# Kernel optimization log

Hardware: AMD Instinct MI355X
Metric: run time of the kernel (lower is better)

## Reference

```python
import jax, jax.numpy as jnp
import numpy as np
from jax import lax

B, S, D, H = 512, 120, 216, 1024
MAX_LEN = 24


def setup_inputs() -> dict:
    key = jax.random.key(0)
    ks = jax.random.split(key, 8)
    u = lambda k, shape: jax.random.uniform(k, shape, jnp.float32, -0.08, 0.08)  # init_weights
    return {
        "src": jax.random.normal(ks[0], (B, S, D), jnp.float32),
        "W_ih": u(ks[1], (4 * H, D)),
        "W_hh": u(ks[2], (4 * H, H)),
        "b_ih": u(ks[3], (4 * H,)),
        "b_hh": u(ks[4], (4 * H,)),
        "W_out": u(ks[5], (D, H)),
        "b_out": u(ks[6], (D,)),
        "max_len": MAX_LEN,
    }


def _lstm_cell(x, h, c, W_ih, W_hh, b):
    # PyTorch gate order: i, f, g, o
    gates = x @ W_ih.T + h @ W_hh.T + b  # (B, 4H)
    i, f, g, o = jnp.split(gates, 4, axis=-1)
    c_new = jax.nn.sigmoid(f) * c + jax.nn.sigmoid(i) * jnp.tanh(g)
    h_new = jax.nn.sigmoid(o) * jnp.tanh(c_new)
    return h_new, c_new


def reference(src, W_ih, W_hh, b_ih, b_hh, W_out, b_out, max_len):
    # Eval-mode forward: dropout off; encoder teacher-forced over src;
    b = b_ih + b_hh
    src_t = jnp.swapaxes(src, 0, 1)  # (S, B, D)
    Bsz = src.shape[0]
    Hd = W_hh.shape[1]
    h0 = jnp.zeros((Bsz, Hd), src.dtype)
    c0 = jnp.zeros((Bsz, Hd), src.dtype)

    def enc_step(carry, x_t):
        h, c = carry
        h, c = _lstm_cell(x_t, h, c, W_ih, W_hh, b)
        return (h, c), None

    (h, c), _ = lax.scan(enc_step, (h0, c0), src_t)

    def dec_step(carry, _):
        h, c, inp = carry
        h, c = _lstm_cell(inp, h, c, W_ih, W_hh, b)
        y = h @ W_out.T + b_out  # project_to_output
        return (h, c, y), y

    (_, _, _), ys = lax.scan(dec_step, (h, c, src_t[-1]), None, length=max_len)
    return jnp.swapaxes(ys, 0, 1)  # (B, max_len, D)
```

## Files before the change

### kernel.cpp

```cpp
#include <hip/hip_runtime.h>
#include <cstdint>
#include <cstddef>

#define B_SZ 512
#define S_SZ 120
#define D_SZ 216
#define H_SZ 1024
#define NG   4096
#define DP   256
#define KENC 1280
#define TMAX 24

#define BM 64
#define BN 128
#define BK 64

using bf16_t = __bf16;
using bf16x8 = __attribute__((ext_vector_type(8))) __bf16;
using f32x4  = __attribute__((ext_vector_type(4))) float;

__device__ __forceinline__ void gload16(const void* g, void* l) {
  __builtin_amdgcn_global_load_lds(
      (const __attribute__((address_space(1))) void*)g,
      (__attribute__((address_space(3))) void*)l, 16, 0, 0);
}

__device__ __forceinline__ float fsigmoid(float x) {
  x = fminf(fmaxf(x, -30.f), 30.f);
  return 1.f / (1.f + __expf(-x));
}
__device__ __forceinline__ float ftanh(float x) {
  x = fminf(fmaxf(x, -15.f), 15.f);
  float e = __expf(2.f * x);
  return (e - 1.f) / (e + 1.f);
}

#define BUFB 24576
struct __align__(16) Smem {
  union {
    bf16_t stage[3][(BM + BN) * BK];
    float gate[BM * 129];
  };
};

template <int EPI>
__global__ __launch_bounds__(256, 1) void gemm_step(
    const bf16_t* __restrict__ A1, int sA1, int n1,
    const bf16_t* __restrict__ A2, int sA2, int n2,
    const bf16_t* __restrict__ W, int sW,
    const float* __restrict__ bias,
    float* __restrict__ cbuf, bf16_t* __restrict__ hout,
    const float* __restrict__ addm, bf16_t* __restrict__ outb,
    float* __restrict__ outf)
{
  __shared__ Smem sm;
  const int t    = threadIdx.x;
  const int m0   = blockIdx.y * BM;
  const int n0   = blockIdx.x * BN;
  const int lane = t & 63;
  const int wv   = t >> 6;
  const int wm   = wv >> 1, wn = wv & 1;
  const int fr   = lane & 15;
  const int fq   = lane >> 4;

  f32x4 acc[2][4] = {};

  float bias4[4];
  if (EPI == 1 || EPI == 3) {
#pragma unroll
    for (int j = 0; j < 4; ++j) {
      int col = n0 + wn * 64 + j * 16 + fr;
      bias4[j] = (EPI == 3 && col >= D_SZ) ? 0.f : bias[col];
    }
  }

  const int r0   = t >> 3;
  const int gcol = (((t & 7) ^ (r0 & 7)) * 8);
  char* ldsbase  = (char*)&sm.stage[0][0];
  const int wofs = wv * 1024;

  const bf16_t* pA1 = A1 ? A1 : A2;
  const bf16_t* pA2 = A2 ? A2 : A1;
  const bf16_t* a1p0 = pA1 + (size_t)(m0 + r0) * sA1 + gcol;
  const bf16_t* a1p1 = pA1 + (size_t)(m0 + r0 + 32) * sA1 + gcol;
  const bf16_t* a2p0 = pA2 + (size_t)(m0 + r0) * sA2 + gcol;
  const bf16_t* a2p1 = pA2 + (size_t)(m0 + r0 + 32) * sA2 + gcol;
  const bf16_t* wp0  = W + (size_t)(n0 + r0) * sW + gcol;
  const bf16_t* wp1  = W + (size_t)(n0 + r0 + 32) * sW + gcol;
  const bf16_t* wp2  = W + (size_t)(n0 + r0 + 64) * sW + gcol;
  const bf16_t* wp3  = W + (size_t)(n0 + r0 + 96) * sW + gcol;

  const int nTot = n1 + n2;

  auto stage = [&](int j, int bf) {
    char* Ab = ldsbase + bf * BUFB + wofs;
    char* Bb = ldsbase + bf * BUFB + 8192 + wofs;
    const int k = j * BK;
    const bf16_t *a0, *a1;
    if (j < n1) { a0 = a1p0 + k; a1 = a1p1 + k; }
    else { const int k2 = k - n1 * BK; a0 = a2p0 + k2; a1 = a2p1 + k2; }
    gload16(a0, Ab);
    gload16(a1, Ab + 4096);
    gload16(wp0 + k, Bb);
    gload16(wp1 + k, Bb + 4096);
    gload16(wp2 + k, Bb + 8192);
    gload16(wp3 + k, Bb + 12288);
  };

  const int swz  = fr & 7;
  const int co0  = ((fq) ^ swz) * 16;
  const int co1  = ((4 + fq) ^ swz) * 16;
  const int arow0 = (wm * 32 + fr) * 128;
  const int arow1 = (wm * 32 + 16 + fr) * 128;
  const int brow  = (wn * 64 + fr) * 128;

  auto compute = [&](int bf) {
    const char* Ab = ldsbase + bf * BUFB;
    const char* Bb = Ab + 8192;
#pragma unroll
    for (int kk = 0; kk < 2; ++kk) {
      const int co = kk ? co1 : co0;
      bf16x8 av0 = *(const bf16x8*)(Ab + arow0 + co);
      bf16x8 av1 = *(const bf16x8*)(Ab + arow1 + co);
      bf16x8 bv[4];
#pragma unroll
      for (int j = 0; j < 4; ++j)
        bv[j] = *(const bf16x8*)(Bb + brow + j * 2048 + co);
#pragma unroll
      for (int j = 0; j < 4; ++j) {
        acc[0][j] = __builtin_amdgcn_mfma_f32_16x16x32_bf16(av0, bv[j], acc[0][j], 0, 0, 0);
        acc[1][j] = __builtin_amdgcn_mfma_f32_16x16x32_bf16(av1, bv[j], acc[1][j], 0, 0, 0);
      }
    }
  };

  stage(0, 0);
  if (nTot > 1) stage(1, 1);
  int cb = 0, sb = 2;
  for (int it = 0; it < nTot; ++it) {
    if (it == nTot - 1) {
      asm volatile("s_waitcnt vmcnt(0)" ::: "memory");
    } else {
      asm volatile("s_waitcnt vmcnt(6)" ::: "memory");
    }
    __builtin_amdgcn_s_barrier();
    if (it + 2 < nTot) stage(it + 2, sb);
    sb = (sb == 2) ? 0 : sb + 1;
    compute(cb);
    cb = (cb == 2) ? 0 : cb + 1;
  }
  __syncthreads();

  if (EPI == 1) {
#pragma unroll
    for (int i = 0; i < 2; ++i)
#pragma unroll
      for (int j = 0; j < 4; ++j)
#pragma unroll
        for (int v = 0; v < 4; ++v) {
          int row = wm * 32 + i * 16 + fq * 4 + v;
          int col = wn * 64 + j * 16 + fr;
          sm.gate[row * 129 + col] = acc[i][j][v] + bias4[j];
        }
    __syncthreads();
    const int u0 = n0 >> 2;
#pragma unroll
    for (int itc = 0; itc < 8; ++itc) {
      int ci = itc * 256 + t;
      int brw = ci >> 5;
      int ju  = ci & 31;
      const float* gp = &sm.gate[brw * 129 + ju * 4];
      float iv = fsigmoid(gp[0]);
      float fv = fsigmoid(gp[1]);
      float gv = ftanh(gp[2]);
      float ov = fsigmoid(gp[3]);
      size_t cix = (size_t)(m0 + brw) * H_SZ + (u0 + ju);
      float cn = fv * cbuf[cix] + iv * gv;
      cbuf[cix] = cn;
      hout[cix] = (bf16_t)(ov * ftanh(cn));
    }
  }

  if (EPI == 2) {
#pragma unroll
    for (int i = 0; i < 2; ++i)
#pragma unroll
      for (int j = 0; j < 4; ++j)
#pragma unroll
        for (int v = 0; v < 4; ++v) {
          int gr = m0 + wm * 32 + i * 16 + fq * 4 + v;
          int gc = n0 + wn * 64 + j * 16 + fr;
          int orig = (gr & 3) * H_SZ + (gr >> 2);
          float val = acc[i][j][v] + addm[(size_t)orig * H_SZ + gc];
          outb[(size_t)gr * H_SZ + gc] = (bf16_t)val;
        }
  }

  if (EPI == 3) {
#pragma unroll
    for (int i = 0; i < 2; ++i)
#pragma unroll
      for (int j = 0; j < 4; ++j)
#pragma unroll
        for (int v = 0; v < 4; ++v) {
          int m = m0 + wm * 32 + i * 16 + fq * 4 + v;
          int n = n0 + wn * 64 + j * 16 + fr;
          if (n < D_SZ) {
            int ts = m >> 9;
            int bb = m & 511;
            outf[((size_t)bb * TMAX + ts) * D_SZ + n] = acc[i][j][v] + bias4[j];
          }
        }
  }
}

__global__ void k_convert_src(const float* __restrict__ src, bf16_t* __restrict__ dst) {
  int idx = blockIdx.x * 256 + threadIdx.x;
  int total = S_SZ * B_SZ * DP;
  if (idx >= total) return;
  int d = idx % DP;
  int r = idx / DP;
  int b = r % B_SZ;
  int tt = r / B_SZ;
  float v = (d < D_SZ) ? src[((size_t)b * S_SZ + tt) * D_SZ + d] : 0.f;
  dst[idx] = (bf16_t)v;
}

__global__ void k_build_wcat(const float* __restrict__ Wih, const float* __restrict__ Whh,
                             bf16_t* __restrict__ Wcat) {
  int idx = blockIdx.x * 256 + threadIdx.x;
  if (idx >= NG * KENC) return;
  int k = idx % KENC;
  int r = idx / KENC;
  int o = (r & 3) * H_SZ + (r >> 2);
  float v;
  if (k < D_SZ)      v = Wih[(size_t)o * D_SZ + k];
  else if (k < DP)   v = 0.f;
  else               v = Whh[(size_t)o * H_SZ + (k - DP)];
  Wcat[idx] = (bf16_t)v;
}

__global__ void k_build_wout(const float* __restrict__ Wout, bf16_t* __restrict__ WoutB,
                             bf16_t* __restrict__ WoutT) {
  int idx = blockIdx.x * 256 + threadIdx.x;
  if (idx < 256 * H_SZ) {
    int h = idx % H_SZ, d = idx / H_SZ;
    WoutB[idx] = (bf16_t)((d < D_SZ) ? Wout[(size_t)d * H_SZ + h] : 0.f);
  }
  if (idx < H_SZ * DP) {
    int d = idx % DP, h = idx / DP;
    WoutT[idx] = (bf16_t)((d < D_SZ) ? Wout[(size_t)d * H_SZ + h] : 0.f);
  }
}

__global__ void k_build_bias(const float* __restrict__ bih, const float* __restrict__ bhh,
                             const float* __restrict__ Wih, const float* __restrict__ bout,
                             float* __restrict__ biasE, float* __restrict__ biasD) {
  int r = blockIdx.x * 256 + threadIdx.x;
  if (r >= NG) return;
  int o = (r & 3) * H_SZ + (r >> 2);
  float be = bih[o] + bhh[o];
  biasE[r] = be;
  float s = 0.f;
  const float* wr = Wih + (size_t)o * D_SZ;
  for (int d = 0; d < D_SZ; ++d) s += wr[d] * bout[d];
  biasD[r] = be + s;
}

extern "C" void kernel_launch(void* const* d_in, const int* in_sizes, int n_in,
                              void* d_out, int out_size, void* d_ws, size_t ws_size,
                              hipStream_t stream) {
  const float* src  = (const float*)d_in[0];
  const float* Wih  = (const float*)d_in[1];
  const float* Whh  = (const float*)d_in[2];
  const float* bih  = (const float*)d_in[3];
  const float* bhh  = (const float*)d_in[4];
  const float* Wout = (const float*)d_in[5];
  const float* bout = (const float*)d_in[6];

  char* ws = (char*)d_ws;
  size_t off = 0;
  auto alloc = [&](size_t bytes) {
    void* p = ws + off;
    off = (off + bytes + 255) & ~(size_t)255;
    return p;
  };
  bf16_t* srcbf = (bf16_t*)alloc((size_t)S_SZ * B_SZ * DP * 2);
  bf16_t* Wcat  = (bf16_t*)alloc((size_t)NG * KENC * 2);
  bf16_t* Wdec  = (bf16_t*)alloc((size_t)NG * H_SZ * 2);
  bf16_t* WoutB = (bf16_t*)alloc((size_t)256 * H_SZ * 2);
  bf16_t* WoutT = (bf16_t*)alloc((size_t)H_SZ * DP * 2);
  float*  biasE = (float*)alloc((size_t)NG * 4);
  float*  biasD = (float*)alloc((size_t)NG * 4);
  float*  cbuf  = (float*)alloc((size_t)B_SZ * H_SZ * 4);
  bf16_t* hP0   = (bf16_t*)alloc((size_t)B_SZ * H_SZ * 2);
  bf16_t* hP1   = (bf16_t*)alloc((size_t)B_SZ * H_SZ * 2);
  bf16_t* Hs    = (bf16_t*)alloc((size_t)TMAX * B_SZ * H_SZ * 2);

  hipMemsetAsync(cbuf, 0, (size_t)B_SZ * H_SZ * 4, stream);
  hipMemsetAsync(hP0, 0, (size_t)B_SZ * H_SZ * 2, stream);

  k_convert_src<<<(S_SZ * B_SZ * DP + 255) / 256, 256, 0, stream>>>(src, srcbf);
  k_build_wcat<<<(NG * KENC + 255) / 256, 256, 0, stream>>>(Wih, Whh, Wcat);
  k_build_wout<<<1024, 256, 0, stream>>>(Wout, WoutB, WoutT);
  k_build_bias<<<(NG + 255) / 256, 256, 0, stream>>>(bih, bhh, Wih, bout, biasE, biasD);

  gemm_step<2><<<dim3(H_SZ / BN, NG / BM), 256, 0, stream>>>(
      Wcat, KENC, DP / BK, nullptr, 0, 0, WoutT, DP,
      nullptr, nullptr, nullptr, Whh, Wdec, nullptr);

  const bf16_t* hprev = hP0;
  for (int s = 0; s < 144; ++s) {
    bf16_t* hnext;
    if (s < 120) hnext = (hprev == hP0) ? hP1 : hP0;
    else         hnext = Hs + (size_t)(s - 120) * B_SZ * H_SZ;
    if (s <= 120) {
      int xi = (s <= 119) ? s : 119;
      gemm_step<1><<<dim3(NG / BN, B_SZ / BM), 256, 0, stream>>>(
          srcbf + (size_t)xi * B_SZ * DP, DP, DP / BK,
          hprev, H_SZ, H_SZ / BK,
          Wcat, KENC, biasE, cbuf, hnext,
          nullptr, nullptr, nullptr);
    } else {
      gemm_step<1><<<dim3(NG / BN, B_SZ / BM), 256, 0, stream>>>(
          nullptr, 0, 0, hprev, H_SZ, H_SZ / BK,
          Wdec, H_SZ, biasD, cbuf, hnext,
          nullptr, nullptr, nullptr);
    }
    hprev = hnext;
  }

  gemm_step<3><<<dim3(2, (TMAX * B_SZ) / BM), 256, 0, stream>>>(
      nullptr, 0, 0, Hs, H_SZ, H_SZ / BK, WoutB, H_SZ,
      bout, nullptr, nullptr, nullptr, nullptr, (float*)d_out);
}
```

Baseline: 2.018 ms.

## Fuse recurrent LSTM steps into one persistent cooperative kernel with grid barrier

Replaces 144 per-timestep GEMM+cell launches with a single persistent cooperative kernel of 256 blocks that loops over all timesteps. A global atomic-counter barrier separates steps. The hidden state is stored with system-coherent flags and loaded bypassing caches so it is visible across blocks. This removes kernel launch and drain overhead per step, at the cost of spin-wait barrier latency and uncached h loads.

```diff
diff --git a/kernel.cpp b/kernel.cpp
--- a/kernel.cpp
+++ b/kernel.cpp
@@ -24,6 +24,11 @@
       (const __attribute__((address_space(1))) void*)g,
       (__attribute__((address_space(3))) void*)l, 16, 0, 0);
 }
+__device__ __forceinline__ void gload16c(const void* g, void* l) {
+  __builtin_amdgcn_global_load_lds(
+      (const __attribute__((address_space(1))) void*)g,
+      (__attribute__((address_space(3))) void*)l, 16, 0, 0x11);
+}
 
 __device__ __forceinline__ float fsigmoid(float x) {
   x = fminf(fmaxf(x, -30.f), 30.f);
@@ -42,6 +47,172 @@
     float gate[BM * 129];
   };
 };
+
+__global__ __launch_bounds__(256, 1) void lstm_chain(
+    const bf16_t* __restrict__ srcbf,
+    const bf16_t* __restrict__ Wcat,
+    const bf16_t* __restrict__ Wdec,
+    const float* __restrict__ biasE,
+    const float* __restrict__ biasD,
+    float* __restrict__ cbuf,
+    bf16_t* __restrict__ hA,
+    bf16_t* __restrict__ hB,
+    bf16_t* __restrict__ Hs,
+    unsigned* __restrict__ bar)
+{
+  __shared__ Smem sm;
+  const int t    = threadIdx.x;
+  const int bid  = blockIdx.x;
+  const int n0   = (bid & 31) * BN;
+  const int m0   = (bid >> 5) * BM;
+  const int lane = t & 63;
+  const int wv   = t >> 6;
+  const int wm   = wv >> 1, wn = wv & 1;
+  const int fr   = lane & 15;
+  const int fq   = lane >> 4;
+
+  const int r0   = t >> 3;
+  const int gcol = (((t & 7) ^ (r0 & 7)) * 8);
+  char* ldsbase  = (char*)&sm.stage[0][0];
+  const int wofs = wv * 1024;
+
+  const int swz  = fr & 7;
+  const int co0  = ((fq) ^ swz) * 16;
+  const int co1  = ((4 + fq) ^ swz) * 16;
+  const int arow0 = (wm * 32 + fr) * 128;
+  const int arow1 = (wm * 32 + 16 + fr) * 128;
+  const int brow  = (wn * 64 + fr) * 128;
+  const int u0    = n0 >> 2;
+
+  const bf16_t* hprev = hA;
+  unsigned target = 0;
+
+#pragma clang loop unroll(disable)
+  for (int s = 0; s < 144; ++s) {
+    const bool enc = (s <= 120);
+    const int  xi  = (s < 120) ? s : 119;
+    const bf16_t* A1  = enc ? (srcbf + (size_t)xi * B_SZ * DP) : hprev;
+    const int     sA1 = enc ? DP : H_SZ;
+    const int     n1  = enc ? (DP / BK) : 0;
+    const bf16_t* W   = enc ? Wcat : Wdec;
+    const int     sW  = enc ? KENC : H_SZ;
+    const float*  bias = enc ? biasE : biasD;
+    bf16_t* hnext = (s < 120) ? ((s & 1) ? hA : hB)
+                              : (Hs + (size_t)(s - 120) * B_SZ * H_SZ);
+    const int nTot = n1 + H_SZ / BK;
+
+    float bias4[4];
+#pragma unroll
+    for (int j = 0; j < 4; ++j) bias4[j] = bias[n0 + wn * 64 + j * 16 + fr];
+
+    const bf16_t* a1p0 = A1 + (size_t)(m0 + r0) * sA1 + gcol;
+    const bf16_t* a1p1 = A1 + (size_t)(m0 + r0 + 32) * sA1 + gcol;
+    const bf16_t* a2p0 = hprev + (size_t)(m0 + r0) * H_SZ + gcol;
+    const bf16_t* a2p1 = hprev + (size_t)(m0 + r0 + 32) * H_SZ + gcol;
+    const bf16_t* wp0  = W + (size_t)(n0 + r0) * sW + gcol;
+    const bf16_t* wp1  = W + (size_t)(n0 + r0 + 32) * sW + gcol;
+    const bf16_t* wp2  = W + (size_t)(n0 + r0 + 64) * sW + gcol;
+    const bf16_t* wp3  = W + (size_t)(n0 + r0 + 96) * sW + gcol;
+
+    f32x4 acc[2][4] = {};
+
+    auto stage = [&](int j, int bf) {
+      char* Ab = ldsbase + bf * BUFB + wofs;
+      char* Bb = ldsbase + bf * BUFB + 8192 + wofs;
+      const int k = j * BK;
+      if (j < n1) {
+        gload16(a1p0 + k, Ab);
+        gload16(a1p1 + k, Ab + 4096);
+      } else {
+        const int k2 = k - n1 * BK;
+        gload16c(a2p0 + k2, Ab);
+        gload16c(a2p1 + k2, Ab + 4096);
+      }
+      gload16(wp0 + k, Bb);
+      gload16(wp1 + k, Bb + 4096);
+      gload16(wp2 + k, Bb + 8192);
+      gload16(wp3 + k, Bb + 12288);
+    };
+
+    auto compute = [&](int bf) {
+      const char* Ab = ldsbase + bf * BUFB;
+      const char* Bb = Ab + 8192;
+#pragma unroll
+      for (int kk = 0; kk < 2; ++kk) {
+        const int co = kk ? co1 : co0;
+        bf16x8 av0 = *(const bf16x8*)(Ab + arow0 + co);
+        bf16x8 av1 = *(const bf16x8*)(Ab + arow1 + co);
+        bf16x8 bv[4];
+#pragma unroll
+        for (int j = 0; j < 4; ++j)
+          bv[j] = *(const bf16x8*)(Bb + brow + j * 2048 + co);
+#pragma unroll
+        for (int j = 0; j < 4; ++j) {
+          acc[0][j] = __builtin_amdgcn_mfma_f32_16x16x32_bf16(av0, bv[j], acc[0][j], 0, 0, 0);
+          acc[1][j] = __builtin_amdgcn_mfma_f32_16x16x32_bf16(av1, bv[j], acc[1][j], 0, 0, 0);
+        }
+      }
+    };
+
+    stage(0, 0);
+    stage(1, 1);
+    int cb = 0, sb = 2;
+    for (int it = 0; it < nTot; ++it) {
+      if (it == nTot - 1) {
+        asm volatile("s_waitcnt vmcnt(0)" ::: "memory");
+      } else {
+        asm volatile("s_waitcnt vmcnt(6)" ::: "memory");
+      }
+      __builtin_amdgcn_s_barrier();
+      if (it + 2 < nTot) stage(it + 2, sb);
+      sb = (sb == 2) ? 0 : sb + 1;
+      compute(cb);
+      cb = (cb == 2) ? 0 : cb + 1;
+    }
+    __syncthreads();
+
+#pragma unroll
+    for (int i = 0; i < 2; ++i)
+#pragma unroll
+      for (int j = 0; j < 4; ++j)
+#pragma unroll
+        for (int v = 0; v < 4; ++v) {
+          int row = wm * 32 + i * 16 + fq * 4 + v;
+          int col = wn * 64 + j * 16 + fr;
+          sm.gate[row * 129 + col] = acc[i][j][v] + bias4[j];
+        }
+    __syncthreads();
+#pragma unroll
+    for (int itc = 0; itc < 8; ++itc) {
+      int ci  = itc * 256 + t;
+      int brw = ci >> 5;
+      int ju  = ci & 31;
+      const float* gp = &sm.gate[brw * 129 + ju * 4];
+      float iv = fsigmoid(gp[0]);
+      float fv = fsigmoid(gp[1]);
+      float gv = ftanh(gp[2]);
+      float ov = fsigmoid(gp[3]);
+      size_t cix = (size_t)(m0 + brw) * H_SZ + (u0 + ju);
+      float cn = fv * cbuf[cix] + iv * gv;
+      cbuf[cix] = cn;
+      bf16_t hb = (bf16_t)(ov * ftanh(cn));
+      uint32_t hv32 = (uint32_t)__builtin_bit_cast(uint16_t, hb);
+      asm volatile("global_store_short %0, %1, off sc0 sc1"
+                   :: "v"((uint16_t*)&hnext[cix]), "v"(hv32) : "memory");
+    }
+
+    target += 256;
+    __syncthreads();
+    if (t == 0) {
+      __hip_atomic_fetch_add(bar, 1u, __ATOMIC_RELAXED, __HIP_MEMORY_SCOPE_AGENT);
+      while (__hip_atomic_load(bar, __ATOMIC_RELAXED, __HIP_MEMORY_SCOPE_AGENT) < target)
+        __builtin_amdgcn_s_sleep(2);
+    }
+    __syncthreads();
+
+    hprev = hnext;
+  }
+}
 
 template <int EPI>
 __global__ __launch_bounds__(256, 1) void gemm_step(
@@ -296,9 +467,11 @@
   bf16_t* hP0   = (bf16_t*)alloc((size_t)B_SZ * H_SZ * 2);
   bf16_t* hP1   = (bf16_t*)alloc((size_t)B_SZ * H_SZ * 2);
   bf16_t* Hs    = (bf16_t*)alloc((size_t)TMAX * B_SZ * H_SZ * 2);
+  unsigned* bar = (unsigned*)alloc(256);
 
   hipMemsetAsync(cbuf, 0, (size_t)B_SZ * H_SZ * 4, stream);
   hipMemsetAsync(hP0, 0, (size_t)B_SZ * H_SZ * 2, stream);
+  hipMemsetAsync(bar, 0, 256, stream);
 
   k_convert_src<<<(S_SZ * B_SZ * DP + 255) / 256, 256, 0, stream>>>(src, srcbf);
   k_build_wcat<<<(NG * KENC + 255) / 256, 256, 0, stream>>>(Wih, Whh, Wcat);
@@ -309,25 +482,21 @@
       Wcat, KENC, DP / BK, nullptr, 0, 0, WoutT, DP,
       nullptr, nullptr, nullptr, Whh, Wdec, nullptr);
 
-  const bf16_t* hprev = hP0;
-  for (int s = 0; s < 144; ++s) {
-    bf16_t* hnext;
-    if (s < 120) hnext = (hprev == hP0) ? hP1 : hP0;
-    else         hnext = Hs + (size_t)(s - 120) * B_SZ * H_SZ;
-    if (s <= 120) {
-      int xi = (s <= 119) ? s : 119;
-      gemm_step<1><<<dim3(NG / BN, B_SZ / BM), 256, 0, stream>>>(
-          srcbf + (size_t)xi * B_SZ * DP, DP, DP / BK,
-          hprev, H_SZ, H_SZ / BK,
-          Wcat, KENC, biasE, cbuf, hnext,
-          nullptr, nullptr, nullptr);
-    } else {
-      gemm_step<1><<<dim3(NG / BN, B_SZ / BM), 256, 0, stream>>>(
-          nullptr, 0, 0, hprev, H_SZ, H_SZ / BK,
-          Wdec, H_SZ, biasD, cbuf, hnext,
-          nullptr, nullptr, nullptr);
-    }
-    hprev = hnext;
+  {
+    const bf16_t* a_src = srcbf;
+    const bf16_t* a_wc  = Wcat;
+    const bf16_t* a_wd  = Wdec;
+    const float*  a_bE  = biasE;
+    const float*  a_bD  = biasD;
+    float*        a_cb  = cbuf;
+    bf16_t*       a_hA  = hP0;
+    bf16_t*       a_hB  = hP1;
+    bf16_t*       a_Hs  = Hs;
+    unsigned*     a_bar = bar;
+    void* kargs[] = {&a_src, &a_wc, &a_wd, &a_bE, &a_bD,
+                     &a_cb, &a_hA, &a_hB, &a_Hs, &a_bar};
+    hipLaunchCooperativeKernel((void*)lstm_chain, dim3(256), dim3(256),
+                               kargs, 0, stream);
   }
 
   gemm_step<3><<<dim3(2, (TMAX * B_SZ) / BM), 256, 0, stream>>>(
```

New measurement: 2.554 ms. +26.6%, slower.
